# Optimization experiments

Measured on AMD Instinct MI355X. Metric: run time of the kernel, lower is better.

Reference implementation:

```python
import jax, jax.numpy as jnp
import numpy as np

EPS = 1e-6
NUM_HEADS = 16


def rotate_every_two(x):
    # pairs (x1, x2) -> (-x2, x1), interleaved on last dim
    x1 = x[..., 0::2]
    x2 = x[..., 1::2]
    return jnp.stack((-x2, x1), axis=-1).reshape(x.shape)


def apply_rotary(q, k, sinu_pos):
    # sinu_pos: [1, L, 2*dh]; split into sin/cos halves of size dh, then
    # repeat each element twice along feature dim ('b n -> b (n j)', j=2).
    L = sinu_pos.shape[1]
    sp = sinu_pos.reshape(L, 2, -1)          # [L, 2, dh]
    sin = jnp.repeat(sp[:, 0], 2, axis=-1)   # [L, D]
    cos = jnp.repeat(sp[:, 1], 2, axis=-1)   # [L, D]
    sin = sin[None, :, None, :]              # broadcast over B, H
    cos = cos[None, :, None, :]
    rot = lambda t: t * cos + rotate_every_two(t) * sin
    return rot(q), rot(k)


def softmax_kernel(data, is_query, proj):
    # data: [B, L, H, D], proj: [M, D] -> features [B, L, H, M]
    D = data.shape[-1]
    data_normalizer = D ** -0.25
    ratio = proj.shape[0] ** -0.5
    data_dash = jnp.einsum('blhd,md->blhm', data_normalizer * data, proj)
    diag = jnp.sum(data * data, axis=-1, keepdims=True) * 0.5 * data_normalizer ** 2
    if is_query:
        m = jax.lax.stop_gradient(jnp.max(data_dash, axis=-1, keepdims=True))
    else:
        m = jax.lax.stop_gradient(jnp.max(data_dash, axis=(-2, -1), keepdims=True))
    return ratio * (jnp.exp(data_dash - diag - m) + EPS)


def favor_noncausal(qp, kp, v):
    # qp, kp: [B, L, H, M]; v: [B, L, H, D]
    kvs = jnp.einsum('blhm,blhd->bhmd', kp, v)
    num = jnp.einsum('blhm,bhmd->blhd', qp, kvs)
    ks_sum = jnp.sum(kp, axis=1)                       # [B, H, M]
    den = jnp.einsum('blhm,bhm->blh', qp, ks_sum)      # [B, L, H]
    return num / den[..., None]


def setup_inputs() -> dict:
    key = jax.random.key(0)
    ks = jax.random.split(key, 7)
    B, L, Dm = 2, 4096, 1024
    M, Dh = 256, Dm // NUM_HEADS
    s = 0.02
    x = jax.random.normal(ks[0], (B, L, Dm), jnp.float32)
    Wq = jax.random.normal(ks[1], (Dm, Dm), jnp.float32) * s
    Wk = jax.random.normal(ks[2], (Dm, Dm), jnp.float32) * s
    Wv = jax.random.normal(ks[3], (Dm, Dm), jnp.float32) * s
    Wo = jax.random.normal(ks[4], (Dm, Dm), jnp.float32) * s
    proj = jax.random.normal(ks[5], (M, Dh), jnp.float32)
    sinu_pos = jax.random.normal(ks[6], (1, L, Dh), jnp.float32)
    return {"x": x, "Wq": Wq, "Wk": Wk, "Wv": Wv, "Wo": Wo,
            "proj": proj, "sinu_pos": sinu_pos}


def reference(x, Wq, Wk, Wv, Wo, proj, sinu_pos):
    B, L, Dm = x.shape
    H = NUM_HEADS
    Dh = Dm // H
    q = (x @ Wq).reshape(B, L, H, Dh)
    k = (x @ Wk).reshape(B, L, H, Dh)
    v = (x @ Wv).reshape(B, L, H, Dh)
    q, k = apply_rotary(q, k, sinu_pos)
    qp = softmax_kernel(q, True, proj)   # [B, L, H, M]
    kp = softmax_kernel(k, False, proj)  # [B, L, H, M]
    av = favor_noncausal(qp, kp, v)      # [B, L, H, Dh]
    return av.reshape(B, L, Dm) @ Wo
```

## Files before the change

kernel.cpp:

```cpp
#include <hip/hip_runtime.h>

typedef __attribute__((ext_vector_type(8))) short short8;
typedef __attribute__((ext_vector_type(4))) float f32x4;
typedef unsigned short USHORT;

#define DNORM 0.35355339059327373f
#define AS1(p) ((const __attribute__((address_space(1))) void*)(p))
#define AS3(p) ((__attribute__((address_space(3))) void*)(p))

__device__ __forceinline__ USHORT f2bf(float f) {
  union { float f; unsigned u; } v; v.f = f;
  unsigned r = v.u + 0x7fffu + ((v.u >> 16) & 1u);
  return (USHORT)(r >> 16);
}
__device__ __forceinline__ float bf2f(USHORT u) {
  union { unsigned u; float f; } v; v.u = ((unsigned)u) << 16;
  return v.f;
}
__device__ __forceinline__ unsigned fkey(float f) {
  union { float f; unsigned u; } v; v.f = f;
  return (v.u & 0x80000000u) ? ~v.u : (v.u | 0x80000000u);
}
__device__ __forceinline__ float keyf(unsigned k) {
  union { unsigned u; float f; } v;
  v.u = (k & 0x80000000u) ? (k ^ 0x80000000u) : ~k;
  return v.f;
}

__device__ __forceinline__ void stage_hl16(const float* __restrict__ src,
                                           USHORT* __restrict__ Ah, USHORT* __restrict__ Al,
                                           int r, int kc) {
  float b[16];
  *(float4*)&b[0] = *(const float4*)(src);
  *(float4*)&b[4] = *(const float4*)(src + 4);
  *(float4*)&b[8] = *(const float4*)(src + 8);
  *(float4*)&b[12] = *(const float4*)(src + 12);
  const int swz = (r & 7) << 3;
  unsigned H[8], L[8];
#pragma unroll
  for (int p = 0; p < 8; ++p) {
    USHORT h0 = f2bf(b[2 * p]), h1 = f2bf(b[2 * p + 1]);
    USHORT l0 = f2bf(b[2 * p] - bf2f(h0)), l1 = f2bf(b[2 * p + 1] - bf2f(h1));
    H[p] = (unsigned)h0 | ((unsigned)h1 << 16);
    L[p] = (unsigned)l0 | ((unsigned)l1 << 16);
  }
  *(uint4*)&Ah[r * 64 + (kc ^ swz)] = make_uint4(H[0], H[1], H[2], H[3]);
  *(uint4*)&Ah[r * 64 + ((kc + 8) ^ swz)] = make_uint4(H[4], H[5], H[6], H[7]);
  *(uint4*)&Al[r * 64 + (kc ^ swz)] = make_uint4(L[0], L[1], L[2], L[3]);
  *(uint4*)&Al[r * 64 + ((kc + 8) ^ swz)] = make_uint4(L[4], L[5], L[6], L[7]);
}

__global__ __launch_bounds__(256) void detect_kernel(const USHORT* __restrict__ w,
                                                     int* __restrict__ flag) {
  const int t = threadIdx.x;
  unsigned mx = 0;
#pragma unroll 8
  for (int c = 0; c < 64; ++c) {
    unsigned a = (unsigned)w[c * 256 + t] & 0x7FFFu;
    if (a > mx) mx = a;
  }
  if (mx > 0x4480u) atomicOr(flag, 1);
}

__global__ __launch_bounds__(256) void cvt_x_kernel(const void* __restrict__ xin,
                                                    USHORT* __restrict__ xh,
                                                    USHORT* __restrict__ xl,
                                                    const void* __restrict__ proj,
                                                    const void* __restrict__ sinu,
                                                    USHORT* __restrict__ projc,
                                                    USHORT* __restrict__ sinuc,
                                                    const int* __restrict__ flag) {
  if (blockIdx.x >= 4096) {
    const int i = ((blockIdx.x - 4096) * 256 + threadIdx.x) * 4;
    const int isp = (i < 16384);
    const int off = isp ? i : (i - 16384);
    const void* src = isp ? proj : sinu;
    USHORT* dst = isp ? projc : sinuc;
    if (*flag) {
      float4 v = *(const float4*)((const float*)src + off);
      USHORT a = f2bf(v.x), b = f2bf(v.y), c = f2bf(v.z), d = f2bf(v.w);
      *(uint2*)(dst + off) = make_uint2((unsigned)a | ((unsigned)b << 16),
                                        (unsigned)c | ((unsigned)d << 16));
    } else {
      *(uint2*)(dst + off) = *(const uint2*)((const USHORT*)src + off);
    }
    return;
  }
  const size_t i = ((size_t)blockIdx.x * 256 + threadIdx.x) * 8;
  if (*flag) {
    const float* xf = (const float*)xin;
    float4 a = *(const float4*)(xf + i);
    float4 b = *(const float4*)(xf + i + 4);
    float c[8] = {a.x, a.y, a.z, a.w, b.x, b.y, b.z, b.w};
    unsigned ho[4], lo[4];
#pragma unroll
    for (int j = 0; j < 4; ++j) {
      USHORT h0 = f2bf(c[2 * j]), h1 = f2bf(c[2 * j + 1]);
      USHORT l0 = f2bf(c[2 * j] - bf2f(h0)), l1 = f2bf(c[2 * j + 1] - bf2f(h1));
      ho[j] = (unsigned)h0 | ((unsigned)h1 << 16);
      lo[j] = (unsigned)l0 | ((unsigned)l1 << 16);
    }
    *(uint4*)(xh + i) = make_uint4(ho[0], ho[1], ho[2], ho[3]);
    *(uint4*)(xl + i) = make_uint4(lo[0], lo[1], lo[2], lo[3]);
  } else {
    uint4 u = *(const uint4*)((const USHORT*)xin + i);
    *(uint4*)(xh + i) = u;
    *(uint4*)(xl + i) = make_uint4(0, 0, 0, 0);
  }
}

__global__ __launch_bounds__(256) void transpose_w_kernel(const void* __restrict__ Wq,
                                                          const void* __restrict__ Wk,
                                                          const void* __restrict__ Wv,
                                                          const void* __restrict__ Wo,
                                                          USHORT* __restrict__ wqkvt,
                                                          USHORT* __restrict__ wot,
                                                          const int* __restrict__ flag) {
  __shared__ __align__(16) USHORT tile[64][80];
  const int z = blockIdx.z;
  const void* src = (z == 0) ? Wq : (z == 1) ? Wk : (z == 2) ? Wv : Wo;
  USHORT* dst = (z < 3) ? (wqkvt + (size_t)z * 1048576) : wot;
  const int r0 = blockIdx.y * 64, c0 = blockIdx.x * 64;
  const int t = threadIdx.x;
  const int rr = t >> 2, c4 = (t & 3) * 16;
  if (*flag) {
    const float* s = (const float*)src + (size_t)(r0 + rr) * 1024 + c0 + c4;
#pragma unroll
    for (int i = 0; i < 4; ++i) {
      float4 v = *(const float4*)(s + i * 4);
      tile[rr][c4 + i * 4 + 0] = f2bf(v.x);
      tile[rr][c4 + i * 4 + 1] = f2bf(v.y);
      tile[rr][c4 + i * 4 + 2] = f2bf(v.z);
      tile[rr][c4 + i * 4 + 3] = f2bf(v.w);
    }
  } else {
    const USHORT* s = (const USHORT*)src + (size_t)(r0 + rr) * 1024 + c0 + c4;
    *(uint4*)&tile[rr][c4] = *(const uint4*)s;
    *(uint4*)&tile[rr][c4 + 8] = *(const uint4*)(s + 8);
  }
  __syncthreads();
  USHORT tmp[16];
#pragma unroll
  for (int i = 0; i < 16; ++i) tmp[i] = tile[c4 + i][rr];
  uint4 o0, o1;
  o0.x = (unsigned)tmp[0] | ((unsigned)tmp[1] << 16);
  o0.y = (unsigned)tmp[2] | ((unsigned)tmp[3] << 16);
  o0.z = (unsigned)tmp[4] | ((unsigned)tmp[5] << 16);
  o0.w = (unsigned)tmp[6] | ((unsigned)tmp[7] << 16);
  o1.x = (unsigned)tmp[8] | ((unsigned)tmp[9] << 16);
  o1.y = (unsigned)tmp[10] | ((unsigned)tmp[11] << 16);
  o1.z = (unsigned)tmp[12] | ((unsigned)tmp[13] << 16);
  o1.w = (unsigned)tmp[14] | ((unsigned)tmp[15] << 16);
  USHORT* d = dst + (size_t)(c0 + rr) * 1024 + r0 + c4;
  *(uint4*)d = o0;
  *(uint4*)(d + 8) = o1;
}

template <bool CANSPLIT, bool ROTEPI, bool FLAGOUT>
__global__ __launch_bounds__(256) void gemm_bt(const USHORT* __restrict__ A,
                                               const USHORT* __restrict__ A2,
                                               const USHORT* __restrict__ Bt,
                                               void* __restrict__ Cv,
                                               USHORT* __restrict__ Vb,
                                               const USHORT* __restrict__ sinu,
                                               float* __restrict__ diag_q,
                                               float* __restrict__ diag_k,
                                               int M, int N, int K, int lda, int ldb, int ldc,
                                               int ldv, int NLO, const int* __restrict__ flag) {
  __shared__ __align__(16) USHORT As[8192];
  __shared__ __align__(16) USHORT Bs[8192];
  __shared__ __align__(16) USHORT As2[CANSPLIT ? 8192 : 16];
  const int fl = *flag;
  const int t = threadIdx.x;
  const int lane = t & 63, wave = t >> 6;
  const int lr = lane & 15, lg = lane >> 4;
  const int row0 = blockIdx.y * 128, col0 = blockIdx.x * 128;
  const bool split = CANSPLIT && (fl != 0) && (col0 < NLO);
  const int wr = (wave >> 1) * 64, wc = (wave & 1) * 64;
  f32x4 acc[4][4] = {};
  for (int k0 = 0; k0 < K; k0 += 64) {
#pragma unroll
    for (int c = 0; c < 4; ++c) {
      const int e = c * 256 + t;
      const int r = e >> 3;
      const int ch = (t & 7) ^ (r & 7);
      const size_t goffA = (size_t)(row0 + r) * lda + k0 + ch * 8;
      const size_t goffB = (size_t)(col0 + r) * ldb + k0 + ch * 8;
      __builtin_amdgcn_global_load_lds(AS1(A + goffA), AS3(&As[c * 2048 + wave * 512]), 16, 0, 0);
      __builtin_amdgcn_global_load_lds(AS1(Bt + goffB), AS3(&Bs[c * 2048 + wave * 512]), 16, 0, 0);
      if constexpr (CANSPLIT) {
        if (split)
          __builtin_amdgcn_global_load_lds(AS1(A2 + goffA), AS3(&As2[c * 2048 + wave * 512]), 16, 0, 0);
      }
    }
    __syncthreads();
#pragma unroll
    for (int ks = 0; ks < 2; ++ks) {
      const int koff = ks * 32 + (lg << 3);
      short8 av_[4], bv[4], av2[4];
#pragma unroll
      for (int i = 0; i < 4; ++i) {
        const int ar = wr + i * 16 + lr;
        av_[i] = *(const short8*)&As[ar * 64 + (koff ^ ((ar & 7) << 3))];
      }
#pragma unroll
      for (int j = 0; j < 4; ++j) {
        const int br = wc + j * 16 + lr;
        bv[j] = *(const short8*)&Bs[br * 64 + (koff ^ ((br & 7) << 3))];
      }
      if constexpr (CANSPLIT) {
        if (split) {
#pragma unroll
          for (int i = 0; i < 4; ++i) {
            const int ar = wr + i * 16 + lr;
            av2[i] = *(const short8*)&As2[ar * 64 + (koff ^ ((ar & 7) << 3))];
          }
        }
      }
#pragma unroll
      for (int i = 0; i < 4; ++i)
#pragma unroll
        for (int j = 0; j < 4; ++j) {
          acc[i][j] = __builtin_amdgcn_mfma_f32_16x16x32_bf16(av_[i], bv[j], acc[i][j], 0, 0, 0);
          if constexpr (CANSPLIT) {
            if (split)
              acc[i][j] = __builtin_amdgcn_mfma_f32_16x16x32_bf16(av2[i], bv[j], acc[i][j], 0, 0, 0);
          }
        }
    }
    __syncthreads();
  }
  if constexpr (ROTEPI) {
    if (col0 < NLO) {
      const int G0 = col0 + wc;
      const int which = G0 >> 10;
      const int h = (G0 & 1023) >> 6;
      float* qk = (float*)Cv;
#pragma unroll
      for (int i = 0; i < 4; ++i) {
        float ss[4] = {0.f, 0.f, 0.f, 0.f};
#pragma unroll
        for (int j = 0; j < 4; ++j) {
          const int G = G0 + j * 16 + lr;
          const int d = G & 63;
          const int j2 = d >> 1;
#pragma unroll
          for (int r = 0; r < 4; ++r) {
            const int R = row0 + wr + i * 16 + (lg << 2) + r;
            const int l = R & 4095;
            const float own = acc[i][j][r];
            const float oth = __shfl_xor(own, 1);
            const float s = bf2f(sinu[l * 64 + j2]);
            const float co = bf2f(sinu[l * 64 + 32 + j2]);
            const float ro = (d & 1) ? (own * co + oth * s) : (own * co - oth * s);
            ss[r] += ro * ro;
            qk[(size_t)R * ldc + G] = ro;
          }
        }
#pragma unroll
        for (int r = 0; r < 4; ++r) {
          float v_ = ss[r];
          v_ += __shfl_xor(v_, 1);
          v_ += __shfl_xor(v_, 2);
          v_ += __shfl_xor(v_, 4);
          v_ += __shfl_xor(v_, 8);
          if (lr == 0) {
            const int R = row0 + wr + i * 16 + (lg << 2) + r;
            (which ? diag_k : diag_q)[R * 16 + h] = v_ * 0.0625f;
          }
        }
      }
    } else {
#pragma unroll
      for (int i = 0; i < 4; ++i) {
#pragma unroll
        for (int r = 0; r < 4; ++r) {
          const int row = row0 + wr + i * 16 + (lg << 2) + r;
#pragma unroll
          for (int j = 0; j < 4; ++j) {
            const int col = col0 + wc + j * 16 + lr - NLO;
            Vb[(size_t)row * ldv + col] = f2bf(acc[i][j][r]);
          }
        }
      }
    }
    return;
  }
#pragma unroll
  for (int i = 0; i < 4; ++i) {
#pragma unroll
    for (int r = 0; r < 4; ++r) {
      const int row = row0 + wr + i * 16 + (lg << 2) + r;
#pragma unroll
      for (int j = 0; j < 4; ++j) {
        const int col = col0 + wc + j * 16 + lr;
        const float v = acc[i][j][r];
        if constexpr (FLAGOUT) {
          if (fl) ((float*)Cv)[(size_t)row * ldc + col] = v;
          else ((USHORT*)Cv)[(size_t)row * ldc + col] = f2bf(v);
        } else {
          ((USHORT*)Cv)[(size_t)row * ldc + col] = f2bf(v);
        }
      }
    }
  }
}

__global__ __launch_bounds__(256) void ddk_max_kernel(const float* __restrict__ qkf,
                                                      const USHORT* __restrict__ proj,
                                                      unsigned* __restrict__ mk) {
  __shared__ __align__(16) USHORT Ph[16384];
  __shared__ __align__(16) USHORT Ah[4096], Al[4096];
  const int t = threadIdx.x, lane = t & 63, wave = t >> 6;
  const int lr = lane & 15, lg = lane >> 4;
  const int bh = blockIdx.y, b = bh >> 4, h = bh & 15;
  const size_t grow0 = (size_t)b * 4096 + blockIdx.x * 64;
  {
#pragma unroll
    for (int c = 0; c < 8; ++c)
      *(uint4*)&Ph[t * 64 + ((c ^ (t & 7)) << 3)] = *(const uint4*)(proj + t * 64 + c * 8);
  }
  {
    const int r = t >> 2, kc = (t & 3) * 16;
    stage_hl16(qkf + (grow0 + r) * 2048 + 1024 + h * 64 + kc, Ah, Al, r, kc);
  }
  __syncthreads();
  f32x4 acc[16] = {};
#pragma unroll
  for (int ks = 0; ks < 2; ++ks) {
    const int koff = ks * 32 + (lg << 3);
    const int ar = wave * 16 + lr;
    short8 a_h = *(const short8*)&Ah[ar * 64 + (koff ^ ((ar & 7) << 3))];
    short8 a_l = *(const short8*)&Al[ar * 64 + (koff ^ ((ar & 7) << 3))];
#pragma unroll
    for (int n = 0; n < 16; ++n) {
      const int br = n * 16 + lr;
      short8 b_h = *(const short8*)&Ph[br * 64 + (koff ^ ((br & 7) << 3))];
      acc[n] = __builtin_amdgcn_mfma_f32_16x16x32_bf16(a_h, b_h, acc[n], 0, 0, 0);
      acc[n] = __builtin_amdgcn_mfma_f32_16x16x32_bf16(a_l, b_h, acc[n], 0, 0, 0);
    }
  }
#pragma unroll
  for (int r = 0; r < 4; ++r) {
    float m_ = acc[0][r];
#pragma unroll
    for (int n = 1; n < 16; ++n) m_ = fmaxf(m_, acc[n][r]);
    m_ = fmaxf(m_, __shfl_xor(m_, 1));
    m_ = fmaxf(m_, __shfl_xor(m_, 2));
    m_ = fmaxf(m_, __shfl_xor(m_, 4));
    m_ = fmaxf(m_, __shfl_xor(m_, 8));
    if (lr == 0) {
      const int row = (int)grow0 + wave * 16 + (lg << 2) + r;
      atomicMax(&mk[row], fkey(m_ * DNORM));
    }
  }
}

__global__ __launch_bounds__(256) void kvs_accum_kernel(const float* __restrict__ qkf,
                                                        const USHORT* __restrict__ vb,
                                                        const USHORT* __restrict__ proj,
                                                        const float* __restrict__ diag_k,
                                                        const unsigned* __restrict__ mk,
                                                        float* __restrict__ kvs_ext) {
  __shared__ __align__(16) USHORT Ph[8192];
  __shared__ __align__(16) USHORT Ah[4096], Al[4096];
  __shared__ __align__(16) USHORT KpT[8192];
  __shared__ __align__(16) USHORT Vt[5120];
  const int t = threadIdx.x, lane = t & 63, wave = t >> 6;
  const int lr = lane & 15, lg = lane >> 4;
  const int bh = blockIdx.z, b = bh >> 4, h = bh & 15;
  const int fh = blockIdx.y;
  const int lstart = blockIdx.x * 512;
  {
    const int pr = t >> 1;
    const USHORT* src = proj + (size_t)(fh * 128 + pr) * 64;
#pragma unroll
    for (int c = 0; c < 4; ++c) {
      const int ch = (t & 1) * 4 + c;
      *(uint4*)&Ph[pr * 64 + ((ch ^ (pr & 7)) << 3)] = *(const uint4*)(src + ch * 8);
    }
  }
  if (t < 64) {
#pragma unroll
    for (int r = 64; r < 80; ++r) Vt[r * 64 + t] = (r == 64) ? (USHORT)0x3F80 : (USHORT)0;
  }
  f32x4 acc2[2][5] = {};
  for (int sub = 0; sub < 8; ++sub) {
    const int row0 = lstart + sub * 64;
    const size_t grow0 = (size_t)b * 4096 + row0;
    {
      const int r = t >> 2, kc = (t & 3) * 16;
      stage_hl16(qkf + (grow0 + r) * 2048 + 1024 + h * 64 + kc, Ah, Al, r, kc);
    }
    {
      const int rv = t & 63, dc = (t >> 6) * 16;
      const USHORT* sv = vb + (grow0 + rv) * 1024 + h * 64 + dc;
      uint4 u0 = *(const uint4*)sv;
      uint4 u1 = *(const uint4*)(sv + 8);
      unsigned wsrc[8] = {u0.x, u0.y, u0.z, u0.w, u1.x, u1.y, u1.z, u1.w};
#pragma unroll
      for (int i = 0; i < 8; ++i) {
        const int d0 = dc + 2 * i;
        Vt[d0 * 64 + (rv ^ ((d0 & 7) << 3))] = (USHORT)(wsrc[i] & 0xffff);
        Vt[(d0 + 1) * 64 + (rv ^ (((d0 + 1) & 7) << 3))] = (USHORT)(wsrc[i] >> 16);
      }
    }
    __syncthreads();
    f32x4 acc1[8] = {};
#pragma unroll
    for (int ks = 0; ks < 2; ++ks) {
      const int koff = ks * 32 + (lg << 3);
      const int ar = wave * 16 + lr;
      short8 a_h = *(const short8*)&Ah[ar * 64 + (koff ^ ((ar & 7) << 3))];
      short8 a_l = *(const short8*)&Al[ar * 64 + (koff ^ ((ar & 7) << 3))];
#pragma unroll
      for (int n = 0; n < 8; ++n) {
        const int br = n * 16 + lr;
        short8 b_h = *(const short8*)&Ph[br * 64 + (koff ^ ((br & 7) << 3))];
        acc1[n] = __builtin_amdgcn_mfma_f32_16x16x32_bf16(a_h, b_h, acc1[n], 0, 0, 0);
        acc1[n] = __builtin_amdgcn_mfma_f32_16x16x32_bf16(a_l, b_h, acc1[n], 0, 0, 0);
      }
    }
    const int rbase = wave * 16 + (lg << 2);
    float dg[4], mkr[4];
#pragma unroll
    for (int r = 0; r < 4; ++r) {
      dg[r] = diag_k[(grow0 + rbase + r) * 16 + h];
      mkr[r] = keyf(mk[grow0 + rbase + r]);
    }
#pragma unroll
    for (int n = 0; n < 8; ++n) {
      const int col = n * 16 + lr;
      USHORT pk[4];
#pragma unroll
      for (int r = 0; r < 4; ++r)
        pk[r] = f2bf(__expf(acc1[n][r] * DNORM - dg[r] - mkr[r]) + 1e-6f);
      const unsigned w0 = (unsigned)pk[0] | ((unsigned)pk[1] << 16);
      const unsigned w1 = (unsigned)pk[2] | ((unsigned)pk[3] << 16);
      *(uint2*)&KpT[col * 64 + (rbase ^ ((col & 7) << 3))] = make_uint2(w0, w1);
    }
    __syncthreads();
#pragma unroll
    for (int ks = 0; ks < 2; ++ks) {
      const int koff = ks * 32 + (lg << 3);
      short8 af[2];
#pragma unroll
      for (int i = 0; i < 2; ++i) {
        const int m = wave * 32 + i * 16 + lr;
        af[i] = *(const short8*)&KpT[m * 64 + (koff ^ ((m & 7) << 3))];
      }
#pragma unroll
      for (int c = 0; c < 5; ++c) {
        const int d = c * 16 + lr;
        short8 bv = *(const short8*)&Vt[d * 64 + (koff ^ ((d & 7) << 3))];
#pragma unroll
        for (int i = 0; i < 2; ++i)
          acc2[i][c] = __builtin_amdgcn_mfma_f32_16x16x32_bf16(af[i], bv, acc2[i][c], 0, 0, 0);
      }
    }
    __syncthreads();
  }
  float* basep = kvs_ext + (size_t)bh * 20480 + (size_t)fh * 128 * 80;
#pragma unroll
  for (int i = 0; i < 2; ++i) {
    const int mrow = wave * 32 + i * 16 + (lg << 2);
#pragma unroll
    for (int c = 0; c < 5; ++c) {
      const int col = c * 16 + lr;
      if (c == 4 && lr != 0) continue;
#pragma unroll
      for (int r = 0; r < 4; ++r)
        atomicAdd(basep + (size_t)(mrow + r) * 80 + col, acc2[i][c][r]);
    }
  }
}

__global__ __launch_bounds__(256) void cvt_kvs_kernel(const float* __restrict__ kvs_ext,
                                                      USHORT* __restrict__ kvsT16) {
  const int bh = blockIdx.x;
  const float* src = kvs_ext + (size_t)bh * 20480;
  USHORT* dst = kvsT16 + (size_t)bh * 20480;
  const int m = threadIdx.x;
#pragma unroll 8
  for (int d = 0; d < 80; ++d)
    dst[d * 256 + m] = f2bf(src[m * 80 + d]);
}

__global__ __launch_bounds__(256) void qav_kernel(const float* __restrict__ qkf,
                                                  const USHORT* __restrict__ proj,
                                                  const float* __restrict__ diag_q,
                                                  const USHORT* __restrict__ kvsT16,
                                                  USHORT* __restrict__ avb) {
  __shared__ __align__(16) USHORT smem[36864];
  USHORT* Ph = smem;
  USHORT* Qp = smem;
  USHORT* Ah = smem + 16384;
  USHORT* Al = smem + 20480;
  USHORT* Btl = smem + 16384;
  const int t = threadIdx.x, lane = t & 63, wave = t >> 6;
  const int lr = lane & 15, lg = lane >> 4;
  const int bh = blockIdx.y, b = bh >> 4, h = bh & 15;
  const size_t grow0 = (size_t)b * 4096 + blockIdx.x * 64;
  {
#pragma unroll
    for (int c = 0; c < 8; ++c)
      *(uint4*)&Ph[t * 64 + ((c ^ (t & 7)) << 3)] = *(const uint4*)(proj + t * 64 + c * 8);
  }
  {
    const int r = t >> 2, kc = (t & 3) * 16;
    stage_hl16(qkf + (grow0 + r) * 2048 + h * 64 + kc, Ah, Al, r, kc);
  }
  __syncthreads();
  f32x4 acc1[16] = {};
#pragma unroll
  for (int ks = 0; ks < 2; ++ks) {
    const int koff = ks * 32 + (lg << 3);
    const int ar = wave * 16 + lr;
    short8 a_h = *(const short8*)&Ah[ar * 64 + (koff ^ ((ar & 7) << 3))];
    short8 a_l = *(const short8*)&Al[ar * 64 + (koff ^ ((ar & 7) << 3))];
#pragma unroll
    for (int n = 0; n < 16; ++n) {
      const int br = n * 16 + lr;
      short8 b_h = *(const short8*)&Ph[br * 64 + (koff ^ ((br & 7) << 3))];
      acc1[n] = __builtin_amdgcn_mfma_f32_16x16x32_bf16(a_h, b_h, acc1[n], 0, 0, 0);
      acc1[n] = __builtin_amdgcn_mfma_f32_16x16x32_bf16(a_l, b_h, acc1[n], 0, 0, 0);
    }
  }
  __syncthreads();
  {
    const USHORT* src = kvsT16 + (size_t)bh * 20480;
#pragma unroll
    for (int c = 0; c < 10; ++c) {
      const int e = c * 256 + t;
      const int d = e >> 5, ch = e & 31;
      *(uint4*)&Btl[d * 256 + ((ch ^ (d & 7)) << 3)] = *(const uint4*)(src + d * 256 + ch * 8);
    }
  }
  const int rbase = wave * 16 + (lg << 2);
  float dg[4], mx[4];
#pragma unroll
  for (int r = 0; r < 4; ++r) dg[r] = diag_q[(grow0 + rbase + r) * 16 + h];
#pragma unroll
  for (int r = 0; r < 4; ++r) {
    float m_ = acc1[0][r];
#pragma unroll
    for (int n = 1; n < 16; ++n) m_ = fmaxf(m_, acc1[n][r]);
    m_ = fmaxf(m_, __shfl_xor(m_, 1));
    m_ = fmaxf(m_, __shfl_xor(m_, 2));
    m_ = fmaxf(m_, __shfl_xor(m_, 4));
    m_ = fmaxf(m_, __shfl_xor(m_, 8));
    mx[r] = m_ * DNORM;
  }
#pragma unroll
  for (int n = 0; n < 16; ++n) {
    const int col = n * 16 + lr;
#pragma unroll
    for (int r = 0; r < 4; ++r) {
      const int row = rbase + r;
      Qp[row * 256 + (col ^ ((row & 7) << 3))] =
          f2bf(__expf(acc1[n][r] * DNORM - dg[r] - mx[r]) + 1e-6f);
    }
  }
  __syncthreads();
  f32x4 acc2[5] = {};
#pragma unroll
  for (int ks2 = 0; ks2 < 8; ++ks2) {
    const int koff = ks2 * 32 + (lg << 3);
    const int ar = wave * 16 + lr;
    short8 a = *(const short8*)&Qp[ar * 256 + (koff ^ ((ar & 7) << 3))];
#pragma unroll
    for (int c = 0; c < 5; ++c) {
      const int cr = c * 16 + lr;
      short8 bv = *(const short8*)&Btl[cr * 256 + (koff ^ ((cr & 7) << 3))];
      acc2[c] = __builtin_amdgcn_mfma_f32_16x16x32_bf16(a, bv, acc2[c], 0, 0, 0);
    }
  }
#pragma unroll
  for (int r = 0; r < 4; ++r) {
    const float den = __shfl(acc2[4][r], (lane & 48));
#pragma unroll
    for (int c = 0; c < 4; ++c) {
      const float o = acc2[c][r] / den;
      avb[(grow0 + rbase + r) * 1024 + h * 64 + c * 16 + lr] = f2bf(o);
    }
  }
}

extern "C" void kernel_launch(void* const* d_in, const int* in_sizes, int n_in,
                              void* d_out, int out_size, void* d_ws, size_t ws_size,
                              hipStream_t stream) {
  char* ws = (char*)d_ws;

  const size_t OFF_FLAG = 0;
  const size_t OFF_WQKVT = 256;
  const size_t OFF_WOT = OFF_WQKVT + 6291456;
  const size_t OFF_PROJC = OFF_WOT + 2097152;
  const size_t OFF_SINUC = OFF_PROJC + 32768;
  const size_t OFF_XH = OFF_SINUC + 524288;
  const size_t OFF_XL = OFF_XH + 16777216;
  const size_t OFF_QKF = OFF_XL + 16777216;
  const size_t OFF_VB = OFF_QKF + 67108864;
  const size_t OFF_DIAGQ = OFF_VB + 16777216;
  const size_t OFF_DIAGK = OFF_DIAGQ + 524288;
  const size_t OFF_MK = OFF_DIAGK + 524288;
  const size_t OFF_KVS = OFF_MK + 32768;
  const size_t OFF_KVST = OFF_KVS + 2621440;

  int* flag = (int*)(ws + OFF_FLAG);
  USHORT* wqkvt = (USHORT*)(ws + OFF_WQKVT);
  USHORT* wot = (USHORT*)(ws + OFF_WOT);
  USHORT* projc = (USHORT*)(ws + OFF_PROJC);
  USHORT* sinuc = (USHORT*)(ws + OFF_SINUC);
  USHORT* xh = (USHORT*)(ws + OFF_XH);
  USHORT* xl = (USHORT*)(ws + OFF_XL);
  USHORT* avb = (USHORT*)(ws + OFF_XH);
  float* qkf = (float*)(ws + OFF_QKF);
  USHORT* vb = (USHORT*)(ws + OFF_VB);
  float* diagq = (float*)(ws + OFF_DIAGQ);
  float* diagk = (float*)(ws + OFF_DIAGK);
  unsigned* mk = (unsigned*)(ws + OFF_MK);
  float* kvsb = (float*)(ws + OFF_KVS);
  USHORT* kvst = (USHORT*)(ws + OFF_KVST);

  hipMemsetAsync(ws + OFF_FLAG, 0, 256, stream);
  hipMemsetAsync(ws + OFF_MK, 0, 32768, stream);
  hipMemsetAsync(ws + OFF_KVS, 0, 2621440, stream);

  detect_kernel<<<1, 256, 0, stream>>>((const USHORT*)d_in[1], flag);
  cvt_x_kernel<<<4368, 256, 0, stream>>>(d_in[0], xh, xl, d_in[5], d_in[6], projc, sinuc, flag);
  transpose_w_kernel<<<dim3(16, 16, 4), 256, 0, stream>>>(d_in[1], d_in[2], d_in[3], d_in[4],
                                                          wqkvt, wot, flag);
  gemm_bt<true, true, false><<<dim3(24, 64), 256, 0, stream>>>(
      xh, xl, wqkvt, qkf, vb, sinuc, diagq, diagk,
      8192, 3072, 1024, 1024, 1024, 2048, 1024, 2048, flag);
  ddk_max_kernel<<<dim3(64, 32), 256, 0, stream>>>(qkf, projc, mk);
  kvs_accum_kernel<<<dim3(8, 2, 32), 256, 0, stream>>>(qkf, vb, projc, diagk, mk, kvsb);
  cvt_kvs_kernel<<<32, 256, 0, stream>>>(kvsb, kvst);
  qav_kernel<<<dim3(64, 32), 256, 0, stream>>>(qkf, projc, diagq, kvst, avb);
  gemm_bt<false, false, true><<<dim3(8, 64), 256, 0, stream>>>(
      avb, nullptr, wot, d_out, nullptr, nullptr, nullptr, nullptr,
      8192, 1024, 1024, 1024, 1024, 1024, 0, 0, flag);
}
```

Before: 273.2 us.

## Drop split-bf16 low part for x in QK projection and remap GEMM tiles

Removes the hi/lo bf16 split of x used for the Q/K projection columns. This eliminates the xl buffer writes, the extra LDS tile, the extra loads and the doubled MFMA work in the first GEMM. It also adds an XCD-aware block index remap so neighbouring tiles land on the same chiplet for better L2 reuse. The cost is lower precision in Q and K, which feed the exponentials of the softmax kernel and may increase error.

```diff
diff --git a/kernel.cpp b/kernel.cpp
--- a/kernel.cpp
+++ b/kernel.cpp
@@ -64,7 +64,6 @@
 
 __global__ __launch_bounds__(256) void cvt_x_kernel(const void* __restrict__ xin,
                                                     USHORT* __restrict__ xh,
-                                                    USHORT* __restrict__ xl,
                                                     const void* __restrict__ proj,
                                                     const void* __restrict__ sinu,
                                                     USHORT* __restrict__ projc,
@@ -92,20 +91,16 @@
     float4 a = *(const float4*)(xf + i);
     float4 b = *(const float4*)(xf + i + 4);
     float c[8] = {a.x, a.y, a.z, a.w, b.x, b.y, b.z, b.w};
-    unsigned ho[4], lo[4];
+    unsigned ho[4];
 #pragma unroll
     for (int j = 0; j < 4; ++j) {
       USHORT h0 = f2bf(c[2 * j]), h1 = f2bf(c[2 * j + 1]);
-      USHORT l0 = f2bf(c[2 * j] - bf2f(h0)), l1 = f2bf(c[2 * j + 1] - bf2f(h1));
       ho[j] = (unsigned)h0 | ((unsigned)h1 << 16);
-      lo[j] = (unsigned)l0 | ((unsigned)l1 << 16);
     }
     *(uint4*)(xh + i) = make_uint4(ho[0], ho[1], ho[2], ho[3]);
-    *(uint4*)(xl + i) = make_uint4(lo[0], lo[1], lo[2], lo[3]);
   } else {
     uint4 u = *(const uint4*)((const USHORT*)xin + i);
     *(uint4*)(xh + i) = u;
-    *(uint4*)(xl + i) = make_uint4(0, 0, 0, 0);
   }
 }
 
@@ -156,9 +151,8 @@
   *(uint4*)(d + 8) = o1;
 }
 
-template <bool CANSPLIT, bool ROTEPI, bool FLAGOUT>
+template <bool ROTEPI, bool FLAGOUT>
 __global__ __launch_bounds__(256) void gemm_bt(const USHORT* __restrict__ A,
-                                               const USHORT* __restrict__ A2,
                                                const USHORT* __restrict__ Bt,
                                                void* __restrict__ Cv,
                                                USHORT* __restrict__ Vb,
@@ -169,13 +163,15 @@
                                                int ldv, int NLO, const int* __restrict__ flag) {
   __shared__ __align__(16) USHORT As[8192];
   __shared__ __align__(16) USHORT Bs[8192];
-  __shared__ __align__(16) USHORT As2[CANSPLIT ? 8192 : 16];
   const int fl = *flag;
   const int t = threadIdx.x;
   const int lane = t & 63, wave = t >> 6;
   const int lr = lane & 15, lg = lane >> 4;
-  const int row0 = blockIdx.y * 128, col0 = blockIdx.x * 128;
-  const bool split = CANSPLIT && (fl != 0) && (col0 < NLO);
+  const int nwg = gridDim.x * gridDim.y;
+  const int orig = blockIdx.y * gridDim.x + blockIdx.x;
+  const int tile = (orig & 7) * (nwg >> 3) + (orig >> 3);
+  const int bx = tile % gridDim.x, by = tile / gridDim.x;
+  const int row0 = by * 128, col0 = bx * 128;
   const int wr = (wave >> 1) * 64, wc = (wave & 1) * 64;
   f32x4 acc[4][4] = {};
   for (int k0 = 0; k0 < K; k0 += 64) {
@@ -188,16 +184,12 @@
       const size_t goffB = (size_t)(col0 + r) * ldb + k0 + ch * 8;
       __builtin_amdgcn_global_load_lds(AS1(A + goffA), AS3(&As[c * 2048 + wave * 512]), 16, 0, 0);
       __builtin_amdgcn_global_load_lds(AS1(Bt + goffB), AS3(&Bs[c * 2048 + wave * 512]), 16, 0, 0);
-      if constexpr (CANSPLIT) {
-        if (split)
-          __builtin_amdgcn_global_load_lds(AS1(A2 + goffA), AS3(&As2[c * 2048 + wave * 512]), 16, 0, 0);
-      }
     }
     __syncthreads();
 #pragma unroll
     for (int ks = 0; ks < 2; ++ks) {
       const int koff = ks * 32 + (lg << 3);
-      short8 av_[4], bv[4], av2[4];
+      short8 av_[4], bv[4];
 #pragma unroll
       for (int i = 0; i < 4; ++i) {
         const int ar = wr + i * 16 + lr;
@@ -208,25 +200,11 @@
         const int br = wc + j * 16 + lr;
         bv[j] = *(const short8*)&Bs[br * 64 + (koff ^ ((br & 7) << 3))];
       }
-      if constexpr (CANSPLIT) {
-        if (split) {
-#pragma unroll
-          for (int i = 0; i < 4; ++i) {
-            const int ar = wr + i * 16 + lr;
-            av2[i] = *(const short8*)&As2[ar * 64 + (koff ^ ((ar & 7) << 3))];
-          }
-        }
-      }
 #pragma unroll
       for (int i = 0; i < 4; ++i)
 #pragma unroll
-        for (int j = 0; j < 4; ++j) {
+        for (int j = 0; j < 4; ++j)
           acc[i][j] = __builtin_amdgcn_mfma_f32_16x16x32_bf16(av_[i], bv[j], acc[i][j], 0, 0, 0);
-          if constexpr (CANSPLIT) {
-            if (split)
-              acc[i][j] = __builtin_amdgcn_mfma_f32_16x16x32_bf16(av2[i], bv[j], acc[i][j], 0, 0, 0);
-          }
-        }
     }
     __syncthreads();
   }
@@ -612,7 +590,6 @@
   USHORT* projc = (USHORT*)(ws + OFF_PROJC);
   USHORT* sinuc = (USHORT*)(ws + OFF_SINUC);
   USHORT* xh = (USHORT*)(ws + OFF_XH);
-  USHORT* xl = (USHORT*)(ws + OFF_XL);
   USHORT* avb = (USHORT*)(ws + OFF_XH);
   float* qkf = (float*)(ws + OFF_QKF);
   USHORT* vb = (USHORT*)(ws + OFF_VB);
@@ -627,17 +604,17 @@
   hipMemsetAsync(ws + OFF_KVS, 0, 2621440, stream);
 
   detect_kernel<<<1, 256, 0, stream>>>((const USHORT*)d_in[1], flag);
-  cvt_x_kernel<<<4368, 256, 0, stream>>>(d_in[0], xh, xl, d_in[5], d_in[6], projc, sinuc, flag);
+  cvt_x_kernel<<<4368, 256, 0, stream>>>(d_in[0], xh, d_in[5], d_in[6], projc, sinuc, flag);
   transpose_w_kernel<<<dim3(16, 16, 4), 256, 0, stream>>>(d_in[1], d_in[2], d_in[3], d_in[4],
                                                           wqkvt, wot, flag);
-  gemm_bt<true, true, false><<<dim3(24, 64), 256, 0, stream>>>(
-      xh, xl, wqkvt, qkf, vb, sinuc, diagq, diagk,
+  gemm_bt<true, false><<<dim3(24, 64), 256, 0, stream>>>(
+      xh, wqkvt, qkf, vb, sinuc, diagq, diagk,
       8192, 3072, 1024, 1024, 1024, 2048, 1024, 2048, flag);
   ddk_max_kernel<<<dim3(64, 32), 256, 0, stream>>>(qkf, projc, mk);
   kvs_accum_kernel<<<dim3(8, 2, 32), 256, 0, stream>>>(qkf, vb, projc, diagk, mk, kvsb);
   cvt_kvs_kernel<<<32, 256, 0, stream>>>(kvsb, kvst);
   qav_kernel<<<dim3(64, 32), 256, 0, stream>>>(qkf, projc, diagq, kvst, avb);
-  gemm_bt<false, false, true><<<dim3(8, 64), 256, 0, stream>>>(
-      avb, nullptr, wot, d_out, nullptr, nullptr, nullptr, nullptr,
+  gemm_bt<false, true><<<dim3(8, 64), 256, 0, stream>>>(
+      avb, wot, d_out, nullptr, nullptr, nullptr, nullptr,
       8192, 1024, 1024, 1024, 1024, 1024, 0, 0, flag);
 }
```

New measurement: 234.0 us, median of 2. -14.4%, faster.
